# Kernel tuning notes

Hardware: AMD Instinct MI355X
Metric: run time of the kernel (lower is better)

Reference implementation:

```python
import jax, jax.numpy as jnp
import numpy as np
import math

TOP_K = 10  # top-k codes kept by SOHO_Pre_VD for negative sampling
EPS_LN = 1e-5


def layer_norm(x, w, b):
    mu = jnp.mean(x, axis=-1, keepdims=True)
    var = jnp.mean((x - mu) ** 2, axis=-1, keepdims=True)
    return (x - mu) * jax.lax.rsqrt(var + EPS_LN) * w + b


def position_encoding_sine(b, l, d):
    # mask is all-ones [b, l]; identical across batch, compute once and broadcast
    h = w = int(math.sqrt(l))
    ones = jnp.ones((h, w), jnp.float32)
    y_embed = jnp.cumsum(ones, axis=0)
    x_embed = jnp.cumsum(ones, axis=1)
    eps = 1e-6
    two_pi = 2.0 * np.pi
    y_embed = y_embed / (y_embed[-1:, :] + eps) * two_pi
    x_embed = x_embed / (x_embed[:, -1:] + eps) * two_pi
    pf = d // 2
    dim_t = jnp.arange(pf, dtype=jnp.float32)
    dim_t = 10000.0 ** (2.0 * jnp.floor(dim_t / 2.0) / pf)
    px = x_embed[:, :, None] / dim_t  # [h, w, pf]
    py = y_embed[:, :, None] / dim_t
    # interleave sin(even), cos(odd)
    px = jnp.stack([jnp.sin(px[..., 0::2]), jnp.cos(px[..., 1::2])], axis=-1).reshape(h, w, pf)
    py = jnp.stack([jnp.sin(py[..., 0::2]), jnp.cos(py[..., 1::2])], axis=-1).reshape(h, w, pf)
    pos = jnp.concatenate([py, px], axis=-1).reshape(l, d)  # [l, d]
    return jnp.broadcast_to(pos, (b, l, d))


def setup_inputs() -> dict:
    key = jax.random.key(0)
    ks = jax.random.split(key, 10)
    B, L, CIN, D, K = 16, 576, 1024, 768, 8192
    s = 0.02
    return {
        "img": jax.random.normal(ks[0], (B, L, CIN), jnp.float32),
        "mask_indices": jax.random.randint(ks[1], (B, 1), 0, L),
        "lin_w": jax.random.normal(ks[2], (D, CIN), jnp.float32) * s,
        "lin_b": jnp.zeros((D,), jnp.float32),
        "ln1_w": jnp.ones((D,), jnp.float32),
        "ln1_b": jnp.zeros((D,), jnp.float32),
        "embed": jax.random.normal(ks[3], (K, D), jnp.float32),
        "pos_w": jax.random.normal(ks[4], (D, D), jnp.float32) * s,
        "pos_b": jnp.zeros((D,), jnp.float32),
        "gate_w": jax.random.normal(ks[5], (2, 2 * D), jnp.float32) * s,
        "gate_b": jnp.zeros((2,), jnp.float32),
        "gate_ln_w": jnp.ones((2,), jnp.float32),
        "gate_ln_b": jnp.zeros((2,), jnp.float32),
        "out_ln_w": jnp.ones((D,), jnp.float32),
        "out_ln_b": jnp.zeros((D,), jnp.float32),
    }


def reference(img, mask_indices, lin_w, lin_b, ln1_w, ln1_b, embed, pos_w, pos_b,
              gate_w, gate_b, gate_ln_w, gate_ln_b, out_ln_w, out_ln_b):
    b, l, _ = img.shape
    d = lin_w.shape[0]
    # self.linear: Linear -> LayerNorm -> ReLU
    xq = jax.nn.relu(layer_norm(img @ lin_w.T + lin_b, ln1_w, ln1_b))  # [b,l,d]
    x = xq.reshape(b * l, d)
    # SOHO VQ: nearest code by L2, straight-through
    d2 = (x * x).sum(-1, keepdims=True) - 2.0 * (x @ embed.T) + (embed * embed).sum(-1)  # [N,K]
    idx = jnp.argmin(d2, axis=-1)  # [N]
    quant = jnp.take(embed, idx, axis=0)
    quantized = x + jax.lax.stop_gradient(quant - x)
    probs = jax.nn.softmax(-d2, axis=-1)
    topk_values, topk_indices = jax.lax.top_k(probs, TOP_K)  # [N,K'],[N,K']
    # pos_align linear
    quantized = quantized @ pos_w.T + pos_b
    emb_pt = quantized.reshape(b, l, d)
    # gated fusion
    g = jnp.concatenate([emb_pt, xq], axis=-1) @ gate_w.T + gate_b  # [b,l,2]
    g = jax.nn.relu(layer_norm(g, gate_ln_w, gate_ln_b))
    score = jax.nn.softmax(g, axis=-1)
    emb_s, img_s = score[..., 0:1], score[..., 1:2]
    emb_pt = emb_pt * emb_s + xq * img_s
    pos = position_encoding_sine(b, l, d)
    # negative index construction (visual_mask is all ones)
    ind = idx.reshape(b, l).astype(jnp.float32)  # [b,l]
    masked_labels = jnp.take_along_axis(ind, mask_indices, axis=1)  # [b,1]
    masked_neg = (ind == masked_labels).astype(jnp.float32)[..., None]  # [b,l,1]
    samp = jax.random.categorical(jax.random.key(42), jnp.log(topk_values))  # [N]
    neg = jnp.take_along_axis(topk_indices, samp[:, None], axis=1).reshape(b, l, 1).astype(jnp.float32)
    neg_at_mask = jnp.take_along_axis(neg[..., 0], mask_indices, axis=1)[..., None]  # [b,1,1]
    neg_idx = neg_at_mask * masked_neg + ind[..., None] * (1.0 - masked_neg)  # [b,l,1]
    neg_idx = neg_idx.reshape(b * l).astype(jnp.int32)
    # one-hot matmul == embedding gather
    neg_q = jnp.take(embed, neg_idx, axis=0).reshape(b, l, d)
    neg_q = neg_q * emb_s + jax.lax.stop_gradient(xq) * img_s
    out_pos = layer_norm(emb_pt + pos, out_ln_w, out_ln_b)
    out_neg = layer_norm(neg_q + pos, out_ln_w, out_ln_b)
    return (out_pos, out_neg)
```

## Files before the change

kernel.cpp:

```cpp
#include <hip/hip_runtime.h>
#include <stdint.h>

#define M_TOT  9216
#define D_     768
#define CIN_   1024
#define KCODE  8192
#define TOPK   10

typedef unsigned short u16;
typedef __bf16 bf16x8 __attribute__((ext_vector_type(8)));
typedef float f32x4 __attribute__((ext_vector_type(4)));


__device__ inline float block_sum(float v, float* red) {
    int t = threadIdx.x;
    red[t] = v;
    __syncthreads();
    #pragma unroll
    for (int s = 128; s > 0; s >>= 1) {
        if (t < s) red[t] += red[t + s];
        __syncthreads();
    }
    float r = red[0];
    __syncthreads();
    return r;
}

__device__ inline unsigned long long umin64(unsigned long long a, unsigned long long b) {
    return (a < b) ? a : b;
}

__device__ inline u16 f2bf(float f) {
    uint32_t u = __float_as_uint(f);
    uint32_t r = (u + 0x7fffu + ((u >> 16) & 1u)) >> 16;
    return (u16)r;
}
__device__ inline float bf2f(u16 h) {
    return __uint_as_float(((uint32_t)h) << 16);
}

__device__ inline unsigned long long shfl_xor_u64(unsigned long long v, int mask) {
    int lo = (int)(uint32_t)v, hi = (int)(uint32_t)(v >> 32);
    lo = __shfl_xor(lo, mask, 64);
    hi = __shfl_xor(hi, mask, 64);
    return ((unsigned long long)(uint32_t)hi << 32) | (uint32_t)lo;
}

#define GLDS(gp, lp) __builtin_amdgcn_global_load_lds( \
    (const __attribute__((address_space(1))) unsigned int*)(gp), \
    (__attribute__((address_space(3))) unsigned int*)(lp), 16, 0, 0)

__global__ __launch_bounds__(256) void k_gemm1_mfma(
    const u16* __restrict__ Ah, const u16* __restrict__ Am, const u16* __restrict__ Al,
    const u16* __restrict__ Bh, const u16* __restrict__ Bm, const u16* __restrict__ Bl,
    const float* __restrict__ bias, float* __restrict__ C)
{
    __shared__ __align__(16) u16 sm[24576];
    const int t = threadIdx.x;
    const int lane = t & 63, wid = t >> 6;
    const int row0 = blockIdx.y * 128, col0 = blockIdx.x * 128;
    const int r16 = lane & 15, kb = lane >> 4;
    const int wr = wid >> 1, wc = wid & 1;
    const int sc = (((lane & 3) ^ ((lane >> 3) & 3))) * 8;
    const int lrow = lane >> 2;
    const int swz = (r16 >> 1) & 3;

    f32x4 acc[4][4];
    #pragma unroll
    for (int mf = 0; mf < 4; ++mf)
        #pragma unroll
        for (int nf = 0; nf < 4; ++nf)
            acc[mf][nf] = (f32x4){0.f, 0.f, 0.f, 0.f};

    for (int k0 = 0; k0 < CIN_; k0 += 32) {
        __syncthreads();
        #pragma unroll
        for (int i = 0; i < 12; ++i) {
            int mat = i >> 1;
            int c = (i & 1) ? wid + 4 : wid;
            const u16* mp = (mat == 0) ? Ah : (mat == 1) ? Am : (mat == 2) ? Al
                          : (mat == 3) ? Bh : (mat == 4) ? Bm : Bl;
            int rbase = (mat < 3) ? row0 : col0;
            const u16* g = mp + (size_t)(rbase + c * 16 + lrow) * CIN_ + k0 + sc;
            GLDS(g, sm + mat * 4096 + c * 512);
        }
        __syncthreads();

        const int slot = (kb ^ swz) * 8;
        bf16x8 bh[4], bm[4], bl[4];
        #pragma unroll
        for (int nf = 0; nf < 4; ++nf) {
            int offb = 12288 + (wc * 64 + nf * 16 + r16) * 32 + slot;
            bh[nf] = *(const bf16x8*)(sm + offb);
            bm[nf] = *(const bf16x8*)(sm + offb + 4096);
            bl[nf] = *(const bf16x8*)(sm + offb + 8192);
        }
        #pragma unroll
        for (int mf = 0; mf < 4; ++mf) {
            int offa = (wr * 64 + mf * 16 + r16) * 32 + slot;
            bf16x8 ah = *(const bf16x8*)(sm + offa);
            bf16x8 am = *(const bf16x8*)(sm + offa + 4096);
            bf16x8 al = *(const bf16x8*)(sm + offa + 8192);
            #pragma unroll
            for (int nf = 0; nf < 4; ++nf) {
                acc[mf][nf] = __builtin_amdgcn_mfma_f32_16x16x32_bf16(ah, bh[nf], acc[mf][nf], 0, 0, 0);
                acc[mf][nf] = __builtin_amdgcn_mfma_f32_16x16x32_bf16(ah, bm[nf], acc[mf][nf], 0, 0, 0);
                acc[mf][nf] = __builtin_amdgcn_mfma_f32_16x16x32_bf16(am, bh[nf], acc[mf][nf], 0, 0, 0);
                acc[mf][nf] = __builtin_amdgcn_mfma_f32_16x16x32_bf16(am, bm[nf], acc[mf][nf], 0, 0, 0);
                acc[mf][nf] = __builtin_amdgcn_mfma_f32_16x16x32_bf16(ah, bl[nf], acc[mf][nf], 0, 0, 0);
                acc[mf][nf] = __builtin_amdgcn_mfma_f32_16x16x32_bf16(al, bh[nf], acc[mf][nf], 0, 0, 0);
            }
        }
    }

    #pragma unroll
    for (int mf = 0; mf < 4; ++mf) {
        #pragma unroll
        for (int q = 0; q < 4; ++q) {
            int m = row0 + wr * 64 + mf * 16 + kb * 4 + q;
            #pragma unroll
            for (int nf = 0; nf < 4; ++nf) {
                int n = col0 + wc * 64 + nf * 16 + r16;
                C[(size_t)m * D_ + n] = acc[mf][nf][q] + bias[n];
            }
        }
    }
}

__global__ __launch_bounds__(256) void k_gemm3_mfma(
    const u16* __restrict__ Eh, const u16* __restrict__ El,
    const u16* __restrict__ Ph, const u16* __restrict__ Pl,
    const unsigned long long* __restrict__ amin,
    const float* __restrict__ bias, float* __restrict__ C)
{
    __shared__ __align__(16) u16 sm[2][16384];
    const int t = threadIdx.x;
    const int lane = t & 63, wid = t >> 6;
    const int row0 = blockIdx.y * 128, col0 = blockIdx.x * 128;
    const int r16 = lane & 15, kb = lane >> 4;
    const int wr = wid >> 1, wc = wid & 1;
    const int sc = (((lane & 3) ^ ((lane >> 3) & 3))) * 8;
    const int lrow = lane >> 2;
    const int swz = (r16 >> 1) & 3;

    const u16* sb = (wid == 0) ? Eh : (wid == 1) ? El : (wid == 2) ? Ph : Pl;
    int grow[8];
    #pragma unroll
    for (int c = 0; c < 8; ++c) {
        int r = ((wid < 2) ? row0 : col0) + c * 16 + lrow;
        grow[c] = (wid < 2) ? (int)(amin[r] & 0xFFFFFFFFull) : r;
    }

    f32x4 acc[4][4];
    #pragma unroll
    for (int mf = 0; mf < 4; ++mf)
        #pragma unroll
        for (int nf = 0; nf < 4; ++nf)
            acc[mf][nf] = (f32x4){0.f, 0.f, 0.f, 0.f};

    auto STAGE = [&](int buf, int k0) {
        u16* dst = sm[buf] + wid * 4096 + lane * 8;
        #pragma unroll
        for (int c = 0; c < 8; ++c)
            GLDS(sb + (size_t)grow[c] * D_ + k0 + sc, dst + c * 512);
    };

    STAGE(0, 0);
    __syncthreads();
    for (int kt = 0; kt < 24; ++kt) {
        int cur = kt & 1;
        if (kt < 23) STAGE(cur ^ 1, (kt + 1) * 32);
        const u16* B = sm[cur];
        const int slot = (kb ^ swz) * 8;
        bf16x8 bh[4], bl[4];
        #pragma unroll
        for (int nf = 0; nf < 4; ++nf) {
            int off = 8192 + (wc * 64 + nf * 16 + r16) * 32 + slot;
            bh[nf] = *(const bf16x8*)(B + off);
            bl[nf] = *(const bf16x8*)(B + off + 4096);
        }
        #pragma unroll
        for (int mf = 0; mf < 4; ++mf) {
            int off = (wr * 64 + mf * 16 + r16) * 32 + slot;
            bf16x8 ah = *(const bf16x8*)(B + off);
            bf16x8 al = *(const bf16x8*)(B + off + 4096);
            #pragma unroll
            for (int nf = 0; nf < 4; ++nf) {
                acc[mf][nf] = __builtin_amdgcn_mfma_f32_16x16x32_bf16(ah, bh[nf], acc[mf][nf], 0, 0, 0);
                acc[mf][nf] = __builtin_amdgcn_mfma_f32_16x16x32_bf16(ah, bl[nf], acc[mf][nf], 0, 0, 0);
                acc[mf][nf] = __builtin_amdgcn_mfma_f32_16x16x32_bf16(al, bh[nf], acc[mf][nf], 0, 0, 0);
            }
        }
        __syncthreads();
    }

    #pragma unroll
    for (int mf = 0; mf < 4; ++mf) {
        #pragma unroll
        for (int q = 0; q < 4; ++q) {
            int m = row0 + wr * 64 + mf * 16 + kb * 4 + q;
            #pragma unroll
            for (int nf = 0; nf < 4; ++nf) {
                int n = col0 + wc * 64 + nf * 16 + r16;
                C[(size_t)m * D_ + n] = acc[mf][nf][q] + bias[n];
            }
        }
    }
}

__global__ __launch_bounds__(256) void k_gemm2_mfma(
    const u16* __restrict__ Xh, const u16* __restrict__ Xl,
    const u16* __restrict__ Eh, const u16* __restrict__ El,
    const float* __restrict__ xsq, const float* __restrict__ esq,
    const int* __restrict__ rowflag, float* __restrict__ d2row,
    unsigned long long* __restrict__ amin)
{
    __shared__ __align__(16) u16 sm[32768];
    const int t = threadIdx.x;
    const int lane = t & 63, wid = t >> 6;
    const int row0 = blockIdx.y * 128, col0 = blockIdx.x * 128;
    const int r16 = lane & 15, kb = lane >> 4;
    const int wr = wid >> 1, wc = wid & 1;

    f32x4 acc[4][4];
    #pragma unroll
    for (int mf = 0; mf < 4; ++mf)
        #pragma unroll
        for (int nf = 0; nf < 4; ++nf)
            acc[mf][nf] = (f32x4){0.f, 0.f, 0.f, 0.f};

    const u16* sb = (wid == 0) ? Xh : (wid == 1) ? Xl : (wid == 2) ? Eh : El;
    const int rbase = (wid < 2) ? row0 : col0;
    const u16* srcb = sb + (size_t)(rbase + (lane >> 3)) * D_
                         + ((lane & 7) ^ (lane >> 3)) * 8;
    u16* dstb = sm + wid * 8192 + lane * 8;

    const int swz = (r16 & 7);
    for (int kt = 0; kt < 12; ++kt) {
        __syncthreads();
        #pragma unroll
        for (int c = 0; c < 16; ++c) {
            GLDS(srcb + kt * 64 + c * 8 * D_, dstb + c * 512);
        }
        __syncthreads();
        #pragma unroll
        for (int h = 0; h < 2; ++h) {
            const int slot = ((h * 4 + kb) ^ swz) * 8;
            bf16x8 bh[4], bl[4];
            #pragma unroll
            for (int nf = 0; nf < 4; ++nf) {
                int off = (wc * 64 + nf * 16 + r16) * 64 + slot;
                bh[nf] = *(const bf16x8*)(sm + 16384 + off);
                bl[nf] = *(const bf16x8*)(sm + 24576 + off);
            }
            #pragma unroll
            for (int mf = 0; mf < 4; ++mf) {
                int off = (wr * 64 + mf * 16 + r16) * 64 + slot;
                bf16x8 ah = *(const bf16x8*)(sm + off);
                bf16x8 al = *(const bf16x8*)(sm + 8192 + off);
                #pragma unroll
                for (int nf = 0; nf < 4; ++nf) {
                    acc[mf][nf] = __builtin_amdgcn_mfma_f32_16x16x32_bf16(ah, bh[nf], acc[mf][nf], 0, 0, 0);
                    acc[mf][nf] = __builtin_amdgcn_mfma_f32_16x16x32_bf16(ah, bl[nf], acc[mf][nf], 0, 0, 0);
                    acc[mf][nf] = __builtin_amdgcn_mfma_f32_16x16x32_bf16(al, bh[nf], acc[mf][nf], 0, 0, 0);
                }
            }
        }
    }

    float esqv[4];
    #pragma unroll
    for (int nf = 0; nf < 4; ++nf)
        esqv[nf] = esq[col0 + wc * 64 + nf * 16 + r16];

    #pragma unroll
    for (int mf = 0; mf < 4; ++mf) {
        #pragma unroll
        for (int q = 0; q < 4; ++q) {
            int m = row0 + wr * 64 + mf * 16 + kb * 4 + q;
            float xsv = xsq[m];
            int rf = rowflag[m];
            unsigned long long best = ~0ull;
            #pragma unroll
            for (int nf = 0; nf < 4; ++nf) {
                int n = col0 + wc * 64 + nf * 16 + r16;
                float d2 = (xsv - 2.0f * acc[mf][nf][q]) + esqv[nf];
                if (rf) d2row[(size_t)(rf - 1) * KCODE + n] = d2;
                unsigned long long key =
                    ((unsigned long long)__float_as_uint(d2) << 32) | (unsigned)n;
                best = umin64(best, key);
            }
            #pragma unroll
            for (int msk = 1; msk < 16; msk <<= 1)
                best = umin64(best, shfl_xor_u64(best, msk));
            if (r16 == 0) atomicMin(&amin[m], best);
        }
    }
}

__global__ __launch_bounds__(256) void k_prep(
    const float* __restrict__ img, u16* __restrict__ Ih, u16* __restrict__ Im,
    u16* __restrict__ Il,
    const float* __restrict__ lin_w, u16* __restrict__ Wh, u16* __restrict__ Wm,
    u16* __restrict__ Wl,
    const float* __restrict__ pos_w, u16* __restrict__ Ph, u16* __restrict__ Pl,
    float* __restrict__ pos,
    const int* __restrict__ mask, int* __restrict__ rowflag)
{
    int bid = blockIdx.x, t = threadIdx.x;
    if (bid < 9216) {
        int i = bid * 256 + t;
        float4 v = ((const float4*)img)[i];
        ushort4 hv, mv, lv;
        float x, r;
        x = v.x; hv.x = f2bf(x); r = x - bf2f(hv.x); mv.x = f2bf(r); lv.x = f2bf(r - bf2f(mv.x));
        x = v.y; hv.y = f2bf(x); r = x - bf2f(hv.y); mv.y = f2bf(r); lv.y = f2bf(r - bf2f(mv.y));
        x = v.z; hv.z = f2bf(x); r = x - bf2f(hv.z); mv.z = f2bf(r); lv.z = f2bf(r - bf2f(mv.z));
        x = v.w; hv.w = f2bf(x); r = x - bf2f(hv.w); mv.w = f2bf(r); lv.w = f2bf(r - bf2f(mv.w));
        ((ushort4*)Ih)[i] = hv; ((ushort4*)Im)[i] = mv; ((ushort4*)Il)[i] = lv;
    } else if (bid < 9984) {
        int i = (bid - 9216) * 256 + t;
        float4 v = ((const float4*)lin_w)[i];
        ushort4 hv, mv, lv;
        float x, r;
        x = v.x; hv.x = f2bf(x); r = x - bf2f(hv.x); mv.x = f2bf(r); lv.x = f2bf(r - bf2f(mv.x));
        x = v.y; hv.y = f2bf(x); r = x - bf2f(hv.y); mv.y = f2bf(r); lv.y = f2bf(r - bf2f(mv.y));
        x = v.z; hv.z = f2bf(x); r = x - bf2f(hv.z); mv.z = f2bf(r); lv.z = f2bf(r - bf2f(mv.z));
        x = v.w; hv.w = f2bf(x); r = x - bf2f(hv.w); mv.w = f2bf(r); lv.w = f2bf(r - bf2f(mv.w));
        ((ushort4*)Wh)[i] = hv; ((ushort4*)Wm)[i] = mv; ((ushort4*)Wl)[i] = lv;
    } else if (bid < 10560) {
        int i = (bid - 9984) * 256 + t;
        float4 v = ((const float4*)pos_w)[i];
        ushort4 hv, lv;
        hv.x = f2bf(v.x); lv.x = f2bf(v.x - bf2f(hv.x));
        hv.y = f2bf(v.y); lv.y = f2bf(v.y - bf2f(hv.y));
        hv.z = f2bf(v.z); lv.z = f2bf(v.z - bf2f(hv.z));
        hv.w = f2bf(v.w); lv.w = f2bf(v.w - bf2f(hv.w));
        ((ushort4*)Ph)[i] = hv; ((ushort4*)Pl)[i] = lv;
    } else if (bid < 11136) {
        int l = bid - 10560;
        for (int k = t; k < D_; k += 256) {
            int kk = (k < 384) ? k : k - 384;
            int m = kk >> 1;
            float coord = (k < 384) ? (float)(l / 24) : (float)(l % 24);
            float v = (coord + 1.0f) / 24.000001f * 6.28318530717958647692f;
            float tm = exp2f((float)m * (13.287712379549449f / 192.0f));
            float a = v / tm;
            pos[(size_t)l * D_ + k] = (kk & 1) ? cosf(a) : sinf(a);
        }
    } else {
        int i = (bid - 11136) * 256 + t;
        int b = i / 576, l = i - b * 576;
        rowflag[i] = (mask[b] == l) ? (b + 1) : 0;
    }
}

__global__ __launch_bounds__(256) void k_ln_esq(
    const float* __restrict__ in, const float* __restrict__ w,
    const float* __restrict__ b, float* __restrict__ xq, float* __restrict__ xsq,
    u16* __restrict__ Xh, u16* __restrict__ Xl,
    const float* __restrict__ E, float* __restrict__ esq,
    u16* __restrict__ Eh, u16* __restrict__ El)
{
    __shared__ float red[256];
    int t = threadIdx.x;
    if (blockIdx.x < 9216) {
        int r = blockIdx.x;
        const float* row = in + (size_t)r * D_;
        float v0 = row[t], v1 = row[t + 256], v2 = row[t + 512];
        float mu = block_sum(v0 + v1 + v2, red) * (1.0f / 768.0f);
        float d0 = v0 - mu, d1 = v1 - mu, d2 = v2 - mu;
        float var = block_sum(d0 * d0 + d1 * d1 + d2 * d2, red) * (1.0f / 768.0f);
        float rn = 1.0f / sqrtf(var + 1e-5f);
        float o0 = fmaxf(0.0f, d0 * rn * w[t] + b[t]);
        float o1 = fmaxf(0.0f, d1 * rn * w[t + 256] + b[t + 256]);
        float o2 = fmaxf(0.0f, d2 * rn * w[t + 512] + b[t + 512]);
        float* orow = xq + (size_t)r * D_;
        orow[t] = o0; orow[t + 256] = o1; orow[t + 512] = o2;
        u16 h0 = f2bf(o0), h1 = f2bf(o1), h2 = f2bf(o2);
        Xh[(size_t)r * D_ + t]       = h0;
        Xh[(size_t)r * D_ + t + 256] = h1;
        Xh[(size_t)r * D_ + t + 512] = h2;
        Xl[(size_t)r * D_ + t]       = f2bf(o0 - bf2f(h0));
        Xl[(size_t)r * D_ + t + 256] = f2bf(o1 - bf2f(h1));
        Xl[(size_t)r * D_ + t + 512] = f2bf(o2 - bf2f(h2));
        float q = block_sum(o0 * o0 + o1 * o1 + o2 * o2, red);
        if (t == 0) xsq[r] = q;
    } else {
        int r = blockIdx.x - 9216;
        const float* row = E + (size_t)r * D_;
        float v0 = row[t], v1 = row[t + 256], v2 = row[t + 512];
        u16 h0 = f2bf(v0), h1 = f2bf(v1), h2 = f2bf(v2);
        Eh[(size_t)r * D_ + t]       = h0;
        Eh[(size_t)r * D_ + t + 256] = h1;
        Eh[(size_t)r * D_ + t + 512] = h2;
        El[(size_t)r * D_ + t]       = f2bf(v0 - bf2f(h0));
        El[(size_t)r * D_ + t + 256] = f2bf(v1 - bf2f(h1));
        El[(size_t)r * D_ + t + 512] = f2bf(v2 - bf2f(h2));
        float s = block_sum(v0 * v0 + v1 * v1 + v2 * v2, red);
        if (t == 0) esq[r] = s;
    }
}

__global__ __launch_bounds__(256) void k_gate(
    const float* __restrict__ embpt, const float* __restrict__ xq,
    const float* __restrict__ gw, const float* __restrict__ gb,
    const float* __restrict__ glnw, const float* __restrict__ glnb,
    float* __restrict__ scores)
{
    __shared__ float red[256];
    int r = blockIdx.x, t = threadIdx.x;
    const float* ep = embpt + (size_t)r * D_;
    const float* xr = xq + (size_t)r * D_;
    float g0 = 0.0f, g1 = 0.0f;
    for (int k = t; k < 1536; k += 256) {
        float v = (k < 768) ? ep[k] : xr[k - 768];
        g0 = fmaf(v, gw[k], g0);
        g1 = fmaf(v, gw[1536 + k], g1);
    }
    g0 = block_sum(g0, red);
    g1 = block_sum(g1, red);
    if (t == 0) {
        g0 += gb[0]; g1 += gb[1];
        float mu = 0.5f * (g0 + g1);
        float h0 = g0 - mu, h1 = g1 - mu;
        float var = 0.5f * (h0 * h0 + h1 * h1);
        float rn = 1.0f / sqrtf(var + 1e-5f);
        float o0 = fmaxf(0.0f, h0 * rn * glnw[0] + glnb[0]);
        float o1 = fmaxf(0.0f, h1 * rn * glnw[1] + glnb[1]);
        float m = fmaxf(o0, o1);
        float e0 = expf(o0 - m), e1 = expf(o1 - m);
        float inv = 1.0f / (e0 + e1);
        scores[r * 2 + 0] = e0 * inv;
        scores[r * 2 + 1] = e1 * inv;
    }
}

__device__ inline void threefry2x32(uint32_t x0, uint32_t x1,
                                    uint32_t& o0, uint32_t& o1)
{
    const uint32_t ks0 = 0u, ks1 = 42u;
    const uint32_t ks2 = ks0 ^ ks1 ^ 0x1BD11BDAu;
    uint32_t ks[3] = {ks0, ks1, ks2};
    x0 += ks[0]; x1 += ks[1];
    const int R0[4] = {13, 15, 26, 6};
    const int R1[4] = {17, 29, 16, 24};
    #pragma unroll
    for (int i = 0; i < 5; ++i) {
        const int* R = (i & 1) ? R1 : R0;
        #pragma unroll
        for (int q = 0; q < 4; ++q) {
            x0 += x1;
            x1 = (x1 << R[q]) | (x1 >> (32 - R[q]));
            x1 ^= x0;
        }
        x0 += ks[(i + 1) % 3];
        x1 += ks[(i + 2) % 3] + (uint32_t)(i + 1);
    }
    o0 = x0; o1 = x1;
}

__global__ __launch_bounds__(256) void k_topk_sample(
    const float* __restrict__ d2row, const unsigned long long* __restrict__ amin,
    const int* __restrict__ mask, int* __restrict__ mlabel, int* __restrict__ negsel)
{
    __shared__ float sd2[KCODE];
    __shared__ unsigned long long rbuf[256];
    __shared__ float rfs[256];
    __shared__ int sel[TOPK];
    __shared__ float selv[TOPK];
    __shared__ float sS;
    int b = blockIdx.x, t = threadIdx.x;
    for (int j = t; j < KCODE; j += 256) sd2[j] = d2row[b * KCODE + j];
    __syncthreads();
    for (int p = 0; p < TOPK; ++p) {
        unsigned long long best = ~0ull;
        for (int j = t; j < KCODE; j += 256) {
            bool skip = false;
            for (int q = 0; q < p; ++q) skip = skip || (j == sel[q]);
            if (skip) continue;
            unsigned long long key =
                ((unsigned long long)__float_as_uint(sd2[j]) << 32) | (unsigned)j;
            best = umin64(best, key);
        }
        rbuf[t] = best;
        __syncthreads();
        for (int s = 128; s > 0; s >>= 1) {
            if (t < s) rbuf[t] = umin64(rbuf[t], rbuf[t + s]);
            __syncthreads();
        }
        if (t == 0) {
            sel[p] = (int)(rbuf[0] & 0xFFFFFFFFull);
            selv[p] = __uint_as_float((uint32_t)(rbuf[0] >> 32));
        }
        __syncthreads();
    }
    float d2min = selv[0];
    float part = 0.0f;
    for (int j = t; j < KCODE; j += 256) part += expf(d2min - sd2[j]);
    part = block_sum(part, rfs);
    if (t == 0) sS = part;
    __syncthreads();
    if (t == 0) {
        int rb = b * 576 + mask[b];
        mlabel[b] = (int)(amin[rb] & 0xFFFFFFFFull);
        float S = sS;
        float bestv = 0.0f;
        int samp = 0;
        bool first = true;
        for (int k = 0; k < TOPK; ++k) {
            float pk = expf(d2min - selv[k]) / S;
            float logit = logf(pk);
            unsigned f = (unsigned)(rb * 10 + k);
            uint32_t o0, o1;
            threefry2x32(0u, f, o0, o1);
            uint32_t bits = o0 ^ o1;
            float uu = __uint_as_float(0x3F800000u | (bits >> 9)) - 1.0f;
            uu = uu + 1.1754944e-38f;
            uu = fmaxf(1.1754944e-38f, uu);
            float gum = -logf(-logf(uu));
            float sc = logit + gum;
            if (first || sc > bestv) { bestv = sc; samp = k; first = false; }
        }
        negsel[b] = sel[samp];
    }
}

__global__ __launch_bounds__(256) void k_final(
    const float* __restrict__ embpt, const float* __restrict__ xq,
    const float* __restrict__ scores, const unsigned long long* __restrict__ amin,
    const int* __restrict__ mlabel, const int* __restrict__ negsel,
    const float* __restrict__ E, const float* __restrict__ pos,
    const float* __restrict__ ow, const float* __restrict__ ob,
    float* __restrict__ outp, float* __restrict__ outn)
{
    __shared__ float red[256];
    int r = blockIdx.x, t = threadIdx.x;
    int b = r / 576, l = r % 576;
    float s0 = scores[r * 2 + 0], s1 = scores[r * 2 + 1];
    int ir = (int)(amin[r] & 0xFFFFFFFFull);
    int nidx = (ir == mlabel[b]) ? negsel[b] : ir;
    const float* ep = embpt + (size_t)r * D_;
    const float* xr = xq + (size_t)r * D_;
    const float* er = E + (size_t)nidx * D_;
    const float* pr = pos + (size_t)l * D_;
    float vp[3], vn[3];
    #pragma unroll
    for (int q = 0; q < 3; ++q) {
        int k = t + q * 256;
        float xv = xr[k] * s1;
        float pv = pr[k];
        vp[q] = (ep[k] * s0 + xv) + pv;
        vn[q] = (er[k] * s0 + xv) + pv;
    }
    float mup = block_sum(vp[0] + vp[1] + vp[2], red) * (1.0f / 768.0f);
    float a0 = vp[0] - mup, a1 = vp[1] - mup, a2 = vp[2] - mup;
    float varp = block_sum(a0 * a0 + a1 * a1 + a2 * a2, red) * (1.0f / 768.0f);
    float rnp = 1.0f / sqrtf(varp + 1e-5f);
    float mun = block_sum(vn[0] + vn[1] + vn[2], red) * (1.0f / 768.0f);
    float c0 = vn[0] - mun, c1 = vn[1] - mun, c2 = vn[2] - mun;
    float varn = block_sum(c0 * c0 + c1 * c1 + c2 * c2, red) * (1.0f / 768.0f);
    float rnn = 1.0f / sqrtf(varn + 1e-5f);
    float* op = outp + (size_t)r * D_;
    float* on = outn + (size_t)r * D_;
    op[t]       = a0 * rnp * ow[t]       + ob[t];
    op[t + 256] = a1 * rnp * ow[t + 256] + ob[t + 256];
    op[t + 512] = a2 * rnp * ow[t + 512] + ob[t + 512];
    on[t]       = c0 * rnn * ow[t]       + ob[t];
    on[t + 256] = c1 * rnn * ow[t + 256] + ob[t + 256];
    on[t + 512] = c2 * rnn * ow[t + 512] + ob[t + 512];
}

extern "C" void kernel_launch(void* const* d_in, const int* in_sizes, int n_in,
                              void* d_out, int out_size, void* d_ws, size_t ws_size,
                              hipStream_t stream)
{
    (void)in_sizes; (void)n_in; (void)out_size; (void)ws_size;
    const float* img    = (const float*)d_in[0];
    const int*   maski  = (const int*)d_in[1];
    const float* lin_w  = (const float*)d_in[2];
    const float* lin_b  = (const float*)d_in[3];
    const float* ln1_w  = (const float*)d_in[4];
    const float* ln1_b  = (const float*)d_in[5];
    const float* embed  = (const float*)d_in[6];
    const float* pos_w  = (const float*)d_in[7];
    const float* pos_b  = (const float*)d_in[8];
    const float* gate_w = (const float*)d_in[9];
    const float* gate_b = (const float*)d_in[10];
    const float* glnw   = (const float*)d_in[11];
    const float* glnb   = (const float*)d_in[12];
    const float* olnw   = (const float*)d_in[13];
    const float* olnb   = (const float*)d_in[14];

    uint8_t* wp = (uint8_t*)d_ws;
    auto alloc = [&](size_t bytes) -> void* {
        void* p = (void*)wp;
        wp += (bytes + 255) & ~(size_t)255;
        return p;
    };
    float* bufA = (float*)alloc((size_t)M_TOT * D_ * 4);
    float* xq   = (float*)alloc((size_t)M_TOT * D_ * 4);
    float* xsq  = (float*)alloc((size_t)M_TOT * 4);
    float* esq  = (float*)alloc((size_t)KCODE * 4);
    unsigned long long* amin = (unsigned long long*)alloc((size_t)M_TOT * 8);
    int*   rowflag = (int*)alloc((size_t)M_TOT * 4);
    float* scores = (float*)alloc((size_t)M_TOT * 2 * 4);
    float* posb   = (float*)alloc((size_t)576 * D_ * 4);
    float* d2row  = (float*)alloc((size_t)16 * KCODE * 4);
    int*   mlab   = (int*)alloc(16 * 4);
    int*   negsel = (int*)alloc(16 * 4);
    u16* Wh = (u16*)alloc((size_t)D_ * CIN_ * 2);
    u16* Wm = (u16*)alloc((size_t)D_ * CIN_ * 2);
    u16* Wl = (u16*)alloc((size_t)D_ * CIN_ * 2);
    u16* Ph = (u16*)alloc((size_t)D_ * D_ * 2);
    u16* Pl = (u16*)alloc((size_t)D_ * D_ * 2);
    u16* R  = (u16*)alloc((size_t)3 * M_TOT * CIN_ * 2);
    u16* Ih = R;
    u16* Im = R + (size_t)M_TOT * CIN_;
    u16* Il = R + (size_t)2 * M_TOT * CIN_;
    u16* Xh = R;
    u16* Xl = Xh + (size_t)M_TOT * D_;
    u16* Eh = Xl + (size_t)M_TOT * D_;
    u16* El = Eh + (size_t)KCODE * D_;

    float* outp = (float*)d_out;
    float* outn = outp + (size_t)M_TOT * D_;

    hipMemsetAsync(amin, 0xFF, M_TOT * sizeof(unsigned long long), stream);

    dim3 blk(256);
    k_prep<<<11172, blk, 0, stream>>>(img, Ih, Im, Il, lin_w, Wh, Wm, Wl,
                                      pos_w, Ph, Pl, posb, maski, rowflag);
    k_gemm1_mfma<<<dim3(D_ / 128, M_TOT / 128), blk, 0, stream>>>(
        Ih, Im, Il, Wh, Wm, Wl, lin_b, bufA);
    k_ln_esq<<<17408, blk, 0, stream>>>(bufA, ln1_w, ln1_b, xq, xsq, Xh, Xl,
                                        embed, esq, Eh, El);
    k_gemm2_mfma<<<dim3(KCODE / 128, M_TOT / 128), blk, 0, stream>>>(
        Xh, Xl, Eh, El, xsq, esq, rowflag, d2row, amin);
    k_gemm3_mfma<<<dim3(D_ / 128, M_TOT / 128), blk, 0, stream>>>(
        Eh, El, Ph, Pl, amin, pos_b, bufA);
    k_gate<<<M_TOT, blk, 0, stream>>>(bufA, xq, gate_w, gate_b, glnw, glnb, scores);
    k_topk_sample<<<16, blk, 0, stream>>>(d2row, amin, maski, mlab, negsel);
    k_final<<<M_TOT, blk, 0, stream>>>(bufA, xq, scores, amin, mlab, negsel,
                                       embed, posb, olnw, olnb, outp, outn);
}
```

Baseline: 747.3 us.

## Retile distance GEMM to 256x256 with 8 waves, double buffering, fused gate

```diff
diff --git a/kernel.cpp b/kernel.cpp
--- a/kernel.cpp
+++ b/kernel.cpp
@@ -208,64 +208,78 @@
     }
 }
 
-__global__ __launch_bounds__(256) void k_gemm2_mfma(
+__global__ __launch_bounds__(512) void k_gemm2_8w(
     const u16* __restrict__ Xh, const u16* __restrict__ Xl,
     const u16* __restrict__ Eh, const u16* __restrict__ El,
     const float* __restrict__ xsq, const float* __restrict__ esq,
     const int* __restrict__ rowflag, float* __restrict__ d2row,
     unsigned long long* __restrict__ amin)
 {
-    __shared__ __align__(16) u16 sm[32768];
-    const int t = threadIdx.x;
-    const int lane = t & 63, wid = t >> 6;
-    const int row0 = blockIdx.y * 128, col0 = blockIdx.x * 128;
+    __shared__ __align__(16) u16 sm[65536];
+    const int tid = threadIdx.x;
+    const int lane = tid & 63, wid = tid >> 6;
+    const int row0 = blockIdx.y * 256, col0 = blockIdx.x * 256;
     const int r16 = lane & 15, kb = lane >> 4;
-    const int wr = wid >> 1, wc = wid & 1;
-
-    f32x4 acc[4][4];
-    #pragma unroll
-    for (int mf = 0; mf < 4; ++mf)
+    const int wr = wid >> 2, wc = wid & 3;
+
+    f32x4 acc[8][4];
+    #pragma unroll
+    for (int mf = 0; mf < 8; ++mf)
         #pragma unroll
         for (int nf = 0; nf < 4; ++nf)
             acc[mf][nf] = (f32x4){0.f, 0.f, 0.f, 0.f};
 
-    const u16* sb = (wid == 0) ? Xh : (wid == 1) ? Xl : (wid == 2) ? Eh : El;
-    const int rbase = (wid < 2) ? row0 : col0;
-    const u16* srcb = sb + (size_t)(rbase + (lane >> 3)) * D_
-                         + ((lane & 7) ^ (lane >> 3)) * 8;
-    u16* dstb = sm + wid * 8192 + lane * 8;
-
-    const int swz = (r16 & 7);
-    for (int kt = 0; kt < 12; ++kt) {
-        __syncthreads();
-        #pragma unroll
-        for (int c = 0; c < 16; ++c) {
-            GLDS(srcb + kt * 64 + c * 8 * D_, dstb + c * 512);
-        }
-        __syncthreads();
+    auto STAGE = [&](int buf, int kt) {
+        const u16* Am = (kt < 24) ? Xh : Xl;
+        const u16* Bm = (kt >= 12 && kt < 24) ? El : Eh;
+        const int kcol = (kt % 12) * 64;
+        u16* base = sm + buf * 32768;
+        #pragma unroll
+        for (int c = 0; c < 4; ++c) {
+            int i = c * 512 + tid;
+            int rr = i >> 3;
+            int kc = (i & 7) ^ (rr & 7);
+            GLDS(Am + (size_t)(row0 + rr) * D_ + kcol + kc * 8, base + i * 8);
+        }
+        #pragma unroll
+        for (int c = 0; c < 4; ++c) {
+            int i = c * 512 + tid;
+            int rr = i >> 3;
+            int kc = (i & 7) ^ (rr & 7);
+            GLDS(Bm + (size_t)(col0 + rr) * D_ + kcol + kc * 8, base + 16384 + i * 8);
+        }
+    };
+
+    STAGE(0, 0);
+    STAGE(1, 1);
+    for (int kt = 0; kt < 36; ++kt) {
+        const int cur = kt & 1;
+        if (kt < 35) asm volatile("s_waitcnt vmcnt(8)" ::: "memory");
+        else         asm volatile("s_waitcnt vmcnt(0)" ::: "memory");
+        __builtin_amdgcn_s_barrier();
+        const u16* Bb = sm + cur * 32768;
         #pragma unroll
         for (int h = 0; h < 2; ++h) {
-            const int slot = ((h * 4 + kb) ^ swz) * 8;
-            bf16x8 bh[4], bl[4];
+            bf16x8 bf[4];
             #pragma unroll
             for (int nf = 0; nf < 4; ++nf) {
-                int off = (wc * 64 + nf * 16 + r16) * 64 + slot;
-                bh[nf] = *(const bf16x8*)(sm + 16384 + off);
-                bl[nf] = *(const bf16x8*)(sm + 24576 + off);
+                int br = wc * 64 + nf * 16 + r16;
+                bf[nf] = *(const bf16x8*)(Bb + 16384 + br * 64
+                                          + (((h * 4 + kb) ^ (br & 7)) * 8));
             }
             #pragma unroll
-            for (int mf = 0; mf < 4; ++mf) {
-                int off = (wr * 64 + mf * 16 + r16) * 64 + slot;
-                bf16x8 ah = *(const bf16x8*)(sm + off);
-                bf16x8 al = *(const bf16x8*)(sm + 8192 + off);
+            for (int mf = 0; mf < 8; ++mf) {
+                int ar = wr * 128 + mf * 16 + r16;
+                bf16x8 af = *(const bf16x8*)(Bb + ar * 64
+                                             + (((h * 4 + kb) ^ (ar & 7)) * 8));
                 #pragma unroll
-                for (int nf = 0; nf < 4; ++nf) {
-                    acc[mf][nf] = __builtin_amdgcn_mfma_f32_16x16x32_bf16(ah, bh[nf], acc[mf][nf], 0, 0, 0);
-                    acc[mf][nf] = __builtin_amdgcn_mfma_f32_16x16x32_bf16(ah, bl[nf], acc[mf][nf], 0, 0, 0);
-                    acc[mf][nf] = __builtin_amdgcn_mfma_f32_16x16x32_bf16(al, bh[nf], acc[mf][nf], 0, 0, 0);
-                }
+                for (int nf = 0; nf < 4; ++nf)
+                    acc[mf][nf] = __builtin_amdgcn_mfma_f32_16x16x32_bf16(
+                        af, bf[nf], acc[mf][nf], 0, 0, 0);
             }
         }
+        __builtin_amdgcn_s_barrier();
+        if (kt + 2 < 36) STAGE(cur, kt + 2);
     }
 
     float esqv[4];
@@ -274,10 +288,10 @@
         esqv[nf] = esq[col0 + wc * 64 + nf * 16 + r16];
 
     #pragma unroll
-    for (int mf = 0; mf < 4; ++mf) {
+    for (int mf = 0; mf < 8; ++mf) {
         #pragma unroll
         for (int q = 0; q < 4; ++q) {
-            int m = row0 + wr * 64 + mf * 16 + kb * 4 + q;
+            int m = row0 + wr * 128 + mf * 16 + kb * 4 + q;
             float xsv = xsq[m];
             int rf = rowflag[m];
             unsigned long long best = ~0ull;
@@ -402,40 +416,6 @@
     }
 }
 
-__global__ __launch_bounds__(256) void k_gate(
-    const float* __restrict__ embpt, const float* __restrict__ xq,
-    const float* __restrict__ gw, const float* __restrict__ gb,
-    const float* __restrict__ glnw, const float* __restrict__ glnb,
-    float* __restrict__ scores)
-{
-    __shared__ float red[256];
-    int r = blockIdx.x, t = threadIdx.x;
-    const float* ep = embpt + (size_t)r * D_;
-    const float* xr = xq + (size_t)r * D_;
-    float g0 = 0.0f, g1 = 0.0f;
-    for (int k = t; k < 1536; k += 256) {
-        float v = (k < 768) ? ep[k] : xr[k - 768];
-        g0 = fmaf(v, gw[k], g0);
-        g1 = fmaf(v, gw[1536 + k], g1);
-    }
-    g0 = block_sum(g0, red);
-    g1 = block_sum(g1, red);
-    if (t == 0) {
-        g0 += gb[0]; g1 += gb[1];
-        float mu = 0.5f * (g0 + g1);
-        float h0 = g0 - mu, h1 = g1 - mu;
-        float var = 0.5f * (h0 * h0 + h1 * h1);
-        float rn = 1.0f / sqrtf(var + 1e-5f);
-        float o0 = fmaxf(0.0f, h0 * rn * glnw[0] + glnb[0]);
-        float o1 = fmaxf(0.0f, h1 * rn * glnw[1] + glnb[1]);
-        float m = fmaxf(o0, o1);
-        float e0 = expf(o0 - m), e1 = expf(o1 - m);
-        float inv = 1.0f / (e0 + e1);
-        scores[r * 2 + 0] = e0 * inv;
-        scores[r * 2 + 1] = e1 * inv;
-    }
-}
-
 __device__ inline void threefry2x32(uint32_t x0, uint32_t x1,
                                     uint32_t& o0, uint32_t& o1)
 {
@@ -526,22 +506,50 @@
     }
 }
 
-__global__ __launch_bounds__(256) void k_final(
+__global__ __launch_bounds__(256) void k_gate_final(
     const float* __restrict__ embpt, const float* __restrict__ xq,
-    const float* __restrict__ scores, const unsigned long long* __restrict__ amin,
+    const unsigned long long* __restrict__ amin,
     const int* __restrict__ mlabel, const int* __restrict__ negsel,
     const float* __restrict__ E, const float* __restrict__ pos,
+    const float* __restrict__ gw, const float* __restrict__ gb,
+    const float* __restrict__ glnw, const float* __restrict__ glnb,
     const float* __restrict__ ow, const float* __restrict__ ob,
     float* __restrict__ outp, float* __restrict__ outn)
 {
     __shared__ float red[256];
+    __shared__ float ss0, ss1;
     int r = blockIdx.x, t = threadIdx.x;
     int b = r / 576, l = r % 576;
-    float s0 = scores[r * 2 + 0], s1 = scores[r * 2 + 1];
+    const float* ep = embpt + (size_t)r * D_;
+    const float* xr = xq + (size_t)r * D_;
+
+    float g0 = 0.0f, g1 = 0.0f;
+    for (int k = t; k < 1536; k += 256) {
+        float v = (k < 768) ? ep[k] : xr[k - 768];
+        g0 = fmaf(v, gw[k], g0);
+        g1 = fmaf(v, gw[1536 + k], g1);
+    }
+    g0 = block_sum(g0, red);
+    g1 = block_sum(g1, red);
+    if (t == 0) {
+        g0 += gb[0]; g1 += gb[1];
+        float mu = 0.5f * (g0 + g1);
+        float h0 = g0 - mu, h1 = g1 - mu;
+        float var = 0.5f * (h0 * h0 + h1 * h1);
+        float rn = 1.0f / sqrtf(var + 1e-5f);
+        float o0 = fmaxf(0.0f, h0 * rn * glnw[0] + glnb[0]);
+        float o1 = fmaxf(0.0f, h1 * rn * glnw[1] + glnb[1]);
+        float m = fmaxf(o0, o1);
+        float e0 = expf(o0 - m), e1 = expf(o1 - m);
+        float inv = 1.0f / (e0 + e1);
+        ss0 = e0 * inv;
+        ss1 = e1 * inv;
+    }
+    __syncthreads();
+    float s0 = ss0, s1 = ss1;
+
     int ir = (int)(amin[r] & 0xFFFFFFFFull);
     int nidx = (ir == mlabel[b]) ? negsel[b] : ir;
-    const float* ep = embpt + (size_t)r * D_;
-    const float* xr = xq + (size_t)r * D_;
     const float* er = E + (size_t)nidx * D_;
     const float* pr = pos + (size_t)l * D_;
     float vp[3], vn[3];
@@ -604,7 +612,6 @@
     float* esq  = (float*)alloc((size_t)KCODE * 4);
     unsigned long long* amin = (unsigned long long*)alloc((size_t)M_TOT * 8);
     int*   rowflag = (int*)alloc((size_t)M_TOT * 4);
-    float* scores = (float*)alloc((size_t)M_TOT * 2 * 4);
     float* posb   = (float*)alloc((size_t)576 * D_ * 4);
     float* d2row  = (float*)alloc((size_t)16 * KCODE * 4);
     int*   mlab   = (int*)alloc(16 * 4);
@@ -635,12 +642,12 @@
         Ih, Im, Il, Wh, Wm, Wl, lin_b, bufA);
     k_ln_esq<<<17408, blk, 0, stream>>>(bufA, ln1_w, ln1_b, xq, xsq, Xh, Xl,
                                         embed, esq, Eh, El);
-    k_gemm2_mfma<<<dim3(KCODE / 128, M_TOT / 128), blk, 0, stream>>>(
+    k_gemm2_8w<<<dim3(KCODE / 256, M_TOT / 256), dim3(512), 0, stream>>>(
         Xh, Xl, Eh, El, xsq, esq, rowflag, d2row, amin);
     k_gemm3_mfma<<<dim3(D_ / 128, M_TOT / 128), blk, 0, stream>>>(
         Eh, El, Ph, Pl, amin, pos_b, bufA);
-    k_gate<<<M_TOT, blk, 0, stream>>>(bufA, xq, gate_w, gate_b, glnw, glnb, scores);
     k_topk_sample<<<16, blk, 0, stream>>>(d2row, amin, maski, mlab, negsel);
-    k_final<<<M_TOT, blk, 0, stream>>>(bufA, xq, scores, amin, mlab, negsel,
-                                       embed, posb, olnw, olnb, outp, outn);
-}
+    k_gate_final<<<M_TOT, blk, 0, stream>>>(bufA, xq, amin, mlab, negsel,
+                                            embed, posb, gate_w, gate_b,
+                                            glnw, glnb, olnw, olnb, outp, outn);
+}
```

Measured after the change: 765.6 us. +2.5%, slower.
